# Performance work log

Hardware: AMD Instinct MI355X
Metric: run time of the kernel (lower is better)

Reference implementation:

```python
import jax, jax.numpy as jnp
import numpy as np

N_NODES = 100000
N_EDGES = 1000000
D_IN = 64
D_OUT = 64


def setup_inputs() -> dict:
    key = jax.random.key(0)
    k1, k2, k3, k4, k5 = jax.random.split(key, 5)
    x = jax.random.normal(k1, (N_NODES, D_IN), dtype=jnp.float32)
    edge_val = jax.random.uniform(k2, (N_EDGES,), dtype=jnp.float32)
    # 'he' initializer: randn(in, out) * sqrt(2/in)
    weight = jax.random.normal(k3, (D_IN, D_OUT), dtype=jnp.float32) * np.sqrt(2.0 / D_IN)
    edge_src = jax.random.randint(k4, (N_EDGES,), 0, N_NODES, dtype=jnp.int32)
    edge_dst = jax.random.randint(k5, (N_EDGES,), 0, N_NODES, dtype=jnp.int32)
    return {"x": x, "edge_val": edge_val, "weight": weight,
            "edge_src": edge_src, "edge_dst": edge_dst}


def reference(x, edge_val, weight, edge_src, edge_dst):
    # order == 'AW': out = A @ x (SpMM over edge list) then @ W
    msgs = edge_val[:, None] * x[edge_src]                      # [E, D_IN]
    agg = jax.ops.segment_sum(msgs, edge_dst, num_segments=N_NODES)  # [N, D_IN]
    out = agg @ weight                                          # [N, D_OUT]
    # embnormalize: F.normalize(out, p=2, dim=1) with eps=1e-12
    norm = jnp.linalg.norm(out, axis=1, keepdims=True)
    out = out / jnp.maximum(norm, 1e-12)
    return jax.nn.relu(out)
```

## Files before the change

### kernel.cpp

```cpp
#include <hip/hip_runtime.h>
#include <hip/hip_fp16.h>

#define D 64

__global__ __launch_bounds__(256) void hist_convert_kernel(
    const int*    __restrict__ edge_dst,
    int*          __restrict__ counts,
    int nEdges,
    const float4* __restrict__ x4,
    uint2*        __restrict__ xhq,
    int nQuads)
{
    const int tid    = blockIdx.x * blockDim.x + threadIdx.x;
    const int stride = gridDim.x * blockDim.x;

    for (int e = tid; e < nEdges; e += stride)
        atomicAdd(&counts[edge_dst[e]], 1);

    for (int q = tid; q < nQuads; q += stride) {
        const float4 v = x4[q];
        const __half2 lo = __floats2half2_rn(v.x, v.y);
        const __half2 hi = __floats2half2_rn(v.z, v.w);
        uint2 u;
        u.x = *reinterpret_cast<const unsigned*>(&lo);
        u.y = *reinterpret_cast<const unsigned*>(&hi);
        xhq[q] = u;
    }
}

__global__ __launch_bounds__(256) void scanA_kernel(
    const int* __restrict__ counts, int* __restrict__ incl,
    int* __restrict__ blockSums, int n)
{
    __shared__ int buf[256];
    const int i = blockIdx.x * 256 + threadIdx.x;
    int v = (i < n) ? counts[i] : 0;
    buf[threadIdx.x] = v;
    __syncthreads();
    for (int off = 1; off < 256; off <<= 1) {
        int t = (threadIdx.x >= off) ? buf[threadIdx.x - off] : 0;
        __syncthreads();
        buf[threadIdx.x] += t;
        __syncthreads();
    }
    if (i < n) incl[i] = buf[threadIdx.x];
    if (threadIdx.x == 255) blockSums[blockIdx.x] = buf[255];
}

__global__ __launch_bounds__(256) void scanC_kernel(
    const int* __restrict__ counts, const int* __restrict__ incl,
    const int* __restrict__ blockSums, int* __restrict__ offsets,
    int* __restrict__ cursor, int n)
{
    __shared__ int red[256];
    const int b = blockIdx.x;
    int p = 0;
    for (int t = threadIdx.x; t < b; t += 256) p += blockSums[t];
    red[threadIdx.x] = p;
    __syncthreads();
    for (int off = 128; off; off >>= 1) {
        if ((int)threadIdx.x < off) red[threadIdx.x] += red[threadIdx.x + off];
        __syncthreads();
    }
    const int prefix = red[0];
    const int i = b * 256 + (int)threadIdx.x;
    if (i < n) {
        const int off = incl[i] - counts[i] + prefix;
        offsets[i] = off;
        cursor[i]  = off;
    }
}

__global__ __launch_bounds__(256) void scatter_kernel(
    const int*   __restrict__ edge_src,
    const int*   __restrict__ edge_dst,
    const float* __restrict__ edge_val,
    int*  __restrict__ cursor,
    int2* __restrict__ sorted_sv,
    int nEdges)
{
    int i = blockIdx.x * blockDim.x + threadIdx.x;
    const int stride = gridDim.x * blockDim.x;
    for (; i < nEdges; i += stride) {
        const int d = edge_dst[i];
        const int pos = atomicAdd(&cursor[d], 1);
        sorted_sv[pos] = make_int2(edge_src[i], __float_as_int(edge_val[i]));
    }
}

__global__ __launch_bounds__(256) void gather_gemv_norm_kernel(
    const __half* __restrict__ xh,
    const float*  __restrict__ W,
    const int*    __restrict__ offsets,
    const int*    __restrict__ counts,
    const int2*   __restrict__ sorted_sv,
    float*        __restrict__ out,
    int nNodes)
{
    __shared__ float Wt[D][D + 4];
    __shared__ float accL[4][D];

    for (int i = threadIdx.x; i < D * D; i += blockDim.x) {
        const int k = i >> 6, j = i & 63;
        Wt[j][k] = W[i];
    }
    __syncthreads();

    const int lane   = threadIdx.x & 63;
    const int w      = threadIdx.x >> 6;
    const int wave   = (blockIdx.x * blockDim.x + threadIdx.x) >> 6;
    const int nWaves = (gridDim.x * blockDim.x) >> 6;

    for (int n = wave; n < nNodes; n += nWaves) {
        const int start = offsets[n];
        const int cnt   = counts[n];

        float a0 = 0.f, a1 = 0.f, a2 = 0.f, a3 = 0.f;
        int j = start;
        const int end4 = start + (cnt & ~3);
        for (; j < end4; j += 4) {
            const int2 e0 = sorted_sv[j + 0];
            const int2 e1 = sorted_sv[j + 1];
            const int2 e2 = sorted_sv[j + 2];
            const int2 e3 = sorted_sv[j + 3];
            a0 += __int_as_float(e0.y) * __half2float(xh[(size_t)e0.x * D + lane]);
            a1 += __int_as_float(e1.y) * __half2float(xh[(size_t)e1.x * D + lane]);
            a2 += __int_as_float(e2.y) * __half2float(xh[(size_t)e2.x * D + lane]);
            a3 += __int_as_float(e3.y) * __half2float(xh[(size_t)e3.x * D + lane]);
        }
        const int end = start + cnt;
        for (; j < end; ++j) {
            const int2 e = sorted_sv[j];
            a0 += __int_as_float(e.y) * __half2float(xh[(size_t)e.x * D + lane]);
        }
        const float acc = (a0 + a1) + (a2 + a3);

        accL[w][lane] = acc;

        float o = 0.f;
        #pragma unroll
        for (int k = 0; k < D; k += 4) {
            const float4 wv = *reinterpret_cast<const float4*>(&Wt[lane][k]);
            const float4 av = *reinterpret_cast<const float4*>(&accL[w][k]);
            o += av.x * wv.x + av.y * wv.y + av.z * wv.z + av.w * wv.w;
        }

        float ss = o * o;
        #pragma unroll
        for (int off = 32; off; off >>= 1)
            ss += __shfl_xor(ss, off, 64);
        const float inv = 1.f / fmaxf(sqrtf(ss), 1e-12f);

        out[(size_t)n * D + lane] = fmaxf(o * inv, 0.f);
    }
}

extern "C" void kernel_launch(void* const* d_in, const int* in_sizes, int n_in,
                              void* d_out, int out_size, void* d_ws, size_t ws_size,
                              hipStream_t stream)
{
    const float* x        = (const float*)d_in[0];
    const float* edge_val = (const float*)d_in[1];
    const float* weight   = (const float*)d_in[2];
    const int*   edge_src = (const int*)d_in[3];
    const int*   edge_dst = (const int*)d_in[4];

    const int nNodes = in_sizes[0] / D;
    const int nEdges = in_sizes[1];
    const int nB     = (nNodes + 255) / 256;
    const int nQuads = nNodes * D / 4;

    int*    counts    = (int*)d_ws;
    int*    offsets   = counts  + nNodes;
    int*    cursor    = offsets + nNodes;
    int*    incl      = cursor  + nNodes;
    int*    blockSums = incl    + nNodes;
    int2*   sorted_sv = (int2*)(blockSums + 4096);
    __half* xh        = (__half*)(sorted_sv + nEdges);
    float*  out       = (float*)d_out;

    hipMemsetAsync(counts, 0, (size_t)nNodes * sizeof(int), stream);

    hist_convert_kernel<<<2048, 256, 0, stream>>>(
        edge_dst, counts, nEdges, (const float4*)x, (uint2*)xh, nQuads);

    scanA_kernel<<<nB, 256, 0, stream>>>(counts, incl, blockSums, nNodes);
    scanC_kernel<<<nB, 256, 0, stream>>>(counts, incl, blockSums, offsets, cursor, nNodes);

    scatter_kernel<<<4096, 256, 0, stream>>>(
        edge_src, edge_dst, edge_val, cursor, sorted_sv, nEdges);

    gather_gemv_norm_kernel<<<2048, 256, 0, stream>>>(
        xh, weight, offsets, counts, sorted_sv, out, nNodes);
}
```

Baseline: 296.2 us.

## Fuse CSR build and gather-GEMV pipeline into one cooperative persistent kernel

Replaces the memset plus five separate launches with a single cooperative kernel that uses grid-wide syncs between phases: zero counts, histogram plus fp16 convert, chunk sums, prefix scan, scatter, and gather-GEMV-normalize. The histogram now reads edge_dst as int4. The aim is to remove launch gaps and per-kernel tail drain. The cost is a grid capped at 1024 blocks for all phases, grid.sync overhead, and a redundant per-chunk prefix loop. A multi-kernel fallback runs if the cooperative launch fails.

```diff
diff --git a/kernel.cpp b/kernel.cpp
--- a/kernel.cpp
+++ b/kernel.cpp
@@ -1,22 +1,180 @@
 #include <hip/hip_runtime.h>
 #include <hip/hip_fp16.h>
+#include <hip/hip_cooperative_groups.h>
+
+namespace cg = cooperative_groups;
 
 #define D 64
 
+__global__ __launch_bounds__(256, 4) void fused_graphconv_kernel(
+    const float*  __restrict__ x,
+    const float*  __restrict__ edge_val,
+    const float*  __restrict__ W,
+    const int*    __restrict__ edge_src,
+    const int*    __restrict__ edge_dst,
+    int*    __restrict__ counts,
+    int*    __restrict__ offsets,
+    int*    __restrict__ cursor,
+    int*    __restrict__ chunkSum,
+    int2*   __restrict__ sorted_sv,
+    __half* __restrict__ xh,
+    float*  __restrict__ out,
+    int nNodes, int nEdges)
+{
+    cg::grid_group grid = cg::this_grid();
+
+    __shared__ float Wt[D][D + 4];
+    __shared__ float accL[4][D];
+    __shared__ int   sbuf[256];
+
+    const int t        = threadIdx.x;
+    const int tid      = blockIdx.x * blockDim.x + t;
+    const int nThreads = gridDim.x * blockDim.x;
+
+    for (int i = tid; i < nNodes; i += nThreads) counts[i] = 0;
+    grid.sync();
+
+    {
+        const int nE4 = nEdges >> 2;
+        const int4* ed4 = (const int4*)edge_dst;
+        for (int q = tid; q < nE4; q += nThreads) {
+            const int4 d4 = ed4[q];
+            atomicAdd(&counts[d4.x], 1);
+            atomicAdd(&counts[d4.y], 1);
+            atomicAdd(&counts[d4.z], 1);
+            atomicAdd(&counts[d4.w], 1);
+        }
+        for (int e = (nE4 << 2) + tid; e < nEdges; e += nThreads)
+            atomicAdd(&counts[edge_dst[e]], 1);
+    }
+    {
+        const float4* x4 = (const float4*)x;
+        uint2* xq = (uint2*)xh;
+        const int nQ = nNodes * D / 4;
+        for (int q = tid; q < nQ; q += nThreads) {
+            const float4 v = x4[q];
+            const __half2 lo = __floats2half2_rn(v.x, v.y);
+            const __half2 hi = __floats2half2_rn(v.z, v.w);
+            uint2 u;
+            u.x = *(const unsigned*)&lo;
+            u.y = *(const unsigned*)&hi;
+            xq[q] = u;
+        }
+    }
+    grid.sync();
+
+    const int nChunks = (nNodes + 255) / 256;
+    for (int c = blockIdx.x; c < nChunks; c += gridDim.x) {
+        const int i = c * 256 + t;
+        sbuf[t] = (i < nNodes) ? counts[i] : 0;
+        __syncthreads();
+        for (int off = 128; off; off >>= 1) {
+            if (t < off) sbuf[t] += sbuf[t + off];
+            __syncthreads();
+        }
+        if (t == 0) chunkSum[c] = sbuf[0];
+        __syncthreads();
+    }
+    grid.sync();
+
+    for (int c = blockIdx.x; c < nChunks; c += gridDim.x) {
+        int p = 0;
+        for (int u = t; u < c; u += 256) p += chunkSum[u];
+        sbuf[t] = p;
+        __syncthreads();
+        for (int off = 128; off; off >>= 1) {
+            if (t < off) sbuf[t] += sbuf[t + off];
+            __syncthreads();
+        }
+        const int prefix = sbuf[0];
+        __syncthreads();
+
+        const int i = c * 256 + t;
+        const int v = (i < nNodes) ? counts[i] : 0;
+        sbuf[t] = v;
+        __syncthreads();
+        for (int off = 1; off < 256; off <<= 1) {
+            const int tv = (t >= off) ? sbuf[t - off] : 0;
+            __syncthreads();
+            sbuf[t] += tv;
+            __syncthreads();
+        }
+        if (i < nNodes) {
+            const int o = prefix + sbuf[t] - v;
+            offsets[i] = o;
+            cursor[i]  = o;
+        }
+        __syncthreads();
+    }
+    grid.sync();
+
+    for (int e = tid; e < nEdges; e += nThreads) {
+        const int d = edge_dst[e];
+        const int pos = atomicAdd(&cursor[d], 1);
+        sorted_sv[pos] = make_int2(edge_src[e], __float_as_int(edge_val[e]));
+    }
+    for (int i = t; i < D * D; i += 256) {
+        const int k = i >> 6, j = i & 63;
+        Wt[j][k] = W[i];
+    }
+    grid.sync();
+
+    const int lane   = t & 63;
+    const int w      = t >> 6;
+    const int wave   = tid >> 6;
+    const int nWaves = nThreads >> 6;
+
+    for (int n = wave; n < nNodes; n += nWaves) {
+        const int start = offsets[n];
+        const int end   = cursor[n];
+
+        float a0 = 0.f, a1 = 0.f, a2 = 0.f, a3 = 0.f;
+        int j = start;
+        const int end4 = start + ((end - start) & ~3);
+        for (; j < end4; j += 4) {
+            const int2 e0 = sorted_sv[j + 0];
+            const int2 e1 = sorted_sv[j + 1];
+            const int2 e2 = sorted_sv[j + 2];
+            const int2 e3 = sorted_sv[j + 3];
+            a0 += __int_as_float(e0.y) * __half2float(xh[(size_t)e0.x * D + lane]);
+            a1 += __int_as_float(e1.y) * __half2float(xh[(size_t)e1.x * D + lane]);
+            a2 += __int_as_float(e2.y) * __half2float(xh[(size_t)e2.x * D + lane]);
+            a3 += __int_as_float(e3.y) * __half2float(xh[(size_t)e3.x * D + lane]);
+        }
+        for (; j < end; ++j) {
+            const int2 e = sorted_sv[j];
+            a0 += __int_as_float(e.y) * __half2float(xh[(size_t)e.x * D + lane]);
+        }
+        const float acc = (a0 + a1) + (a2 + a3);
+
+        accL[w][lane] = acc;
+
+        float o = 0.f;
+        #pragma unroll
+        for (int k = 0; k < D; k += 4) {
+            const float4 wv = *reinterpret_cast<const float4*>(&Wt[lane][k]);
+            const float4 av = *reinterpret_cast<const float4*>(&accL[w][k]);
+            o += av.x * wv.x + av.y * wv.y + av.z * wv.z + av.w * wv.w;
+        }
+
+        float ss = o * o;
+        #pragma unroll
+        for (int off = 32; off; off >>= 1)
+            ss += __shfl_xor(ss, off, 64);
+        const float inv = 1.f / fmaxf(sqrtf(ss), 1e-12f);
+
+        out[(size_t)n * D + lane] = fmaxf(o * inv, 0.f);
+    }
+}
+
 __global__ __launch_bounds__(256) void hist_convert_kernel(
-    const int*    __restrict__ edge_dst,
-    int*          __restrict__ counts,
-    int nEdges,
-    const float4* __restrict__ x4,
-    uint2*        __restrict__ xhq,
-    int nQuads)
+    const int* __restrict__ edge_dst, int* __restrict__ counts, int nEdges,
+    const float4* __restrict__ x4, uint2* __restrict__ xhq, int nQuads)
 {
     const int tid    = blockIdx.x * blockDim.x + threadIdx.x;
     const int stride = gridDim.x * blockDim.x;
-
     for (int e = tid; e < nEdges; e += stride)
         atomicAdd(&counts[edge_dst[e]], 1);
-
     for (int q = tid; q < nQuads; q += stride) {
         const float4 v = x4[q];
         const __half2 lo = __floats2half2_rn(v.x, v.y);
@@ -99,7 +257,6 @@
 {
     __shared__ float Wt[D][D + 4];
     __shared__ float accL[4][D];
-
     for (int i = threadIdx.x; i < D * D; i += blockDim.x) {
         const int k = i >> 6, j = i & 63;
         Wt[j][k] = W[i];
@@ -165,31 +322,54 @@
     const int*   edge_src = (const int*)d_in[3];
     const int*   edge_dst = (const int*)d_in[4];
 
-    const int nNodes = in_sizes[0] / D;
-    const int nEdges = in_sizes[1];
-    const int nB     = (nNodes + 255) / 256;
-    const int nQuads = nNodes * D / 4;
+    int nNodes = in_sizes[0] / D;
+    int nEdges = in_sizes[1];
+    const int nB = (nNodes + 255) / 256;
 
     int*    counts    = (int*)d_ws;
     int*    offsets   = counts  + nNodes;
     int*    cursor    = offsets + nNodes;
     int*    incl      = cursor  + nNodes;
-    int*    blockSums = incl    + nNodes;
-    int2*   sorted_sv = (int2*)(blockSums + 4096);
+    int*    chunkSum  = incl    + nNodes;
+    int2*   sorted_sv = (int2*)(chunkSum + 4096);
     __half* xh        = (__half*)(sorted_sv + nEdges);
     float*  out       = (float*)d_out;
 
-    hipMemsetAsync(counts, 0, (size_t)nNodes * sizeof(int), stream);
-
-    hist_convert_kernel<<<2048, 256, 0, stream>>>(
-        edge_dst, counts, nEdges, (const float4*)x, (uint2*)xh, nQuads);
-
-    scanA_kernel<<<nB, 256, 0, stream>>>(counts, incl, blockSums, nNodes);
-    scanC_kernel<<<nB, 256, 0, stream>>>(counts, incl, blockSums, offsets, cursor, nNodes);
-
-    scatter_kernel<<<4096, 256, 0, stream>>>(
-        edge_src, edge_dst, edge_val, cursor, sorted_sv, nEdges);
-
-    gather_gemv_norm_kernel<<<2048, 256, 0, stream>>>(
-        xh, weight, offsets, counts, sorted_sv, out, nNodes);
-}
+    bool coopDone = false;
+    int blocksPerCU = 0, nCU = 0, dev = 0;
+    (void)hipGetDevice(&dev);
+    hipError_t eo = hipOccupancyMaxActiveBlocksPerMultiprocessor(
+        &blocksPerCU, fused_graphconv_kernel, 256, 0);
+    hipError_t ec = hipDeviceGetAttribute(
+        &nCU, hipDeviceAttributeMultiprocessorCount, dev);
+
+    if (eo == hipSuccess && ec == hipSuccess && blocksPerCU > 0 && nCU > 0) {
+        int grid = blocksPerCU * nCU;
+        if (grid > 1024) grid = 1024;
+        if (grid >= 64) {
+            void* kargs[] = {
+                (void*)&x, (void*)&edge_val, (void*)&weight,
+                (void*)&edge_src, (void*)&edge_dst,
+                (void*)&counts, (void*)&offsets, (void*)&cursor, (void*)&chunkSum,
+                (void*)&sorted_sv, (void*)&xh, (void*)&out,
+                (void*)&nNodes, (void*)&nEdges
+            };
+            hipError_t le = hipLaunchCooperativeKernel(
+                (const void*)fused_graphconv_kernel,
+                dim3(grid), dim3(256), kargs, 0, stream);
+            coopDone = (le == hipSuccess);
+        }
+    }
+
+    if (!coopDone) {
+        (void)hipMemsetAsync(counts, 0, (size_t)nNodes * sizeof(int), stream);
+        hist_convert_kernel<<<2048, 256, 0, stream>>>(
+            edge_dst, counts, nEdges, (const float4*)x, (uint2*)xh, nNodes * D / 4);
+        scanA_kernel<<<nB, 256, 0, stream>>>(counts, incl, chunkSum, nNodes);
+        scanC_kernel<<<nB, 256, 0, stream>>>(counts, incl, chunkSum, offsets, cursor, nNodes);
+        scatter_kernel<<<4096, 256, 0, stream>>>(
+            edge_src, edge_dst, edge_val, cursor, sorted_sv, nEdges);
+        gather_gemv_norm_kernel<<<2048, 256, 0, stream>>>(
+            xh, weight, offsets, counts, sorted_sv, out, nNodes);
+    }
+}
```

Measured after the change: 627.1 us. 112% more time.
